# Optimization experiments

Measured on AMD Instinct MI355X. Metric: run time of the kernel, lower is better.

The kernel has to match this reference:

```python
import jax, jax.numpy as jnp
import numpy as np

B, S, D = 2, 2048, 2048
H, G = 32, 8            # n_heads, n_kv_groups
HD = D // H             # head_dim = 64
GS = H // G             # group_size = 4


def _rope(t, cos, sin):
    # t: (B, h, S, HD); cos/sin: (S, HD), start_pos = 0
    half = t.shape[-1] // 2
    rot = jnp.concatenate([-t[..., half:], t[..., :half]], axis=-1)
    return t * cos[None, None] + rot * sin[None, None]


def setup_inputs() -> dict:
    key = jax.random.key(0)
    ks = jax.random.split(key, 7)
    x = jax.random.normal(ks[0], (B, S, D), jnp.float32)
    cos = jax.random.normal(ks[1], (S, HD), jnp.float32)
    sin = jax.random.normal(ks[2], (S, HD), jnp.float32)
    mask = jnp.zeros((S, S), jnp.bool_)
    Wq = jax.random.normal(ks[3], (D, D), jnp.float32) * 0.02
    Wk = jax.random.normal(ks[4], (G * HD, D), jnp.float32) * 0.02
    Wv = jax.random.normal(ks[5], (G * HD, D), jnp.float32) * 0.02
    Wo = jax.random.normal(ks[6], (D, D), jnp.float32) * 0.02
    return {"x": x, "cos": cos, "sin": sin, "mask": mask,
            "Wq": Wq, "Wk": Wk, "Wv": Wv, "Wo": Wo}


def reference(x, cos, sin, mask, Wq, Wk, Wv, Wo):
    b, s, d = x.shape
    # projections (nn.Linear: y = x @ W.T)
    q = (x @ Wq.T).reshape(b, s, H, HD).transpose(0, 2, 1, 3)   # (b,H,s,HD)
    k = (x @ Wk.T).reshape(b, s, G, HD).transpose(0, 2, 1, 3)   # (b,G,s,HD)
    v = (x @ Wv.T).reshape(b, s, G, HD).transpose(0, 2, 1, 3)   # (b,G,s,HD)
    q = _rope(q, cos, sin)
    k = _rope(k, cos, sin)
    # GQA: heads grouped contiguously per kv group (equivalent to repeat_interleave on kv)
    qg = q.reshape(b, G, GS, s, HD)
    scores = jnp.einsum('bgmsd,bgtd->bgmst', qg, k) / jnp.sqrt(jnp.float32(HD))
    # NOTE: original calls non-inplace masked_fill and DISCARDS the result,
    # so the mask has no effect on the output; reproduced faithfully.
    attn = jax.nn.softmax(scores, axis=-1)
    y = jnp.einsum('bgmst,bgtd->bgmsd', attn, v)
    y = y.reshape(b, H, s, HD).transpose(0, 2, 1, 3).reshape(b, s, d)
    return y @ Wo.T
```

## Files before the change

### kernel.cpp

```cpp
#include <hip/hip_runtime.h>
#include <hip/hip_bf16.h>
#include <stdint.h>

#define B_ 2
#define S_ 2048
#define D_ 2048
#define H_ 32
#define G_ 8
#define HD_ 64
#define KVD (G_*HD_)

typedef unsigned short u16;
typedef unsigned int u32;
typedef __attribute__((ext_vector_type(8))) short s8v;
typedef __attribute__((ext_vector_type(4))) float f4v;
typedef __attribute__((ext_vector_type(4))) unsigned int u4v;

static __device__ __forceinline__ float bf2f(u16 u){ return __uint_as_float(((u32)u)<<16); }
static __device__ __forceinline__ u16 f2bf(float f){
  u32 b = __float_as_uint(f);
  return (u16)((b + 0x7FFFu + ((b>>16)&1u)) >> 16);
}
static __device__ __forceinline__ u32 pk2bf(float a, float b){
  float2 f2 = make_float2(a, b);
  __hip_bfloat162 h = __float22bfloat162_rn(f2);
  return *(u32*)&h;
}

struct CvtArgs {
  const float *x, *wq, *wk, *wv, *wo;
  u16 *xb, *wqkvb, *wob;
};
__global__ void k_cvt5(CvtArgs a){
  const int E0 = 2097152;
  const int E1 = E0 + 1048576;
  const int E2 = E1 + 262144;
  const int E3 = E2 + 262144;
  const int E4 = E3 + 1048576;
  int u = blockIdx.x*blockDim.x + threadIdx.x;
  int stride = gridDim.x*blockDim.x;
  for (; u < E4; u += stride){
    const float* s; u16* d; int off;
    if      (u < E0){ s = a.x;  d = a.xb;               off = u; }
    else if (u < E1){ s = a.wq; d = a.wqkvb;            off = u - E0; }
    else if (u < E2){ s = a.wk; d = a.wqkvb + 4194304;  off = u - E1; }
    else if (u < E3){ s = a.wv; d = a.wqkvb + 5242880;  off = u - E2; }
    else            { s = a.wo; d = a.wob;              off = u - E3; }
    float4 f = *(const float4*)(s + (long)off*4);
    uint2 o;
    o.x = (u32)f2bf(f.x) | ((u32)f2bf(f.y)<<16);
    o.y = (u32)f2bf(f.z) | ((u32)f2bf(f.w)<<16);
    *(uint2*)(d + (long)off*4) = o;
  }
}

template<int MODE>
__global__ __launch_bounds__(256) void k_gemm(const u16* __restrict__ A,
    const u16* __restrict__ Bw,
    void* __restrict__ C, void* __restrict__ C2, void* __restrict__ C3,
    const float* __restrict__ cs, const float* __restrict__ sn,
    int N_unused, int K){
  __shared__ u16 As[128*32];
  __shared__ u16 Bs[128*32];
  const int tid = threadIdx.x;
  const int lane = tid & 63, wid = tid >> 6;
  const int l15 = lane & 15, l4 = lane >> 4;
  const int wr = wid >> 1, wc = wid & 1;
  const long Arow0 = (long)blockIdx.x * 128;
  const long Brow0 = (long)blockIdx.y * 128;
  f4v acc[4][4] = {};
  for (int k0 = 0; k0 < K; k0 += 32){
    if (k0) __syncthreads();
    #pragma unroll
    for (int is = 0; is < 2; ++is){
      int c = (is*4 + wid)*64 + lane;
      int row = c >> 2, slot = c & 3;
      int ko = slot ^ (row & 3);
      const u16* srcA = A + (Arow0 + row)*K + k0 + ko*8;
      const u16* srcB = Bw + (Brow0 + row)*K + k0 + ko*8;
      __builtin_amdgcn_global_load_lds((__attribute__((address_space(1))) void*)(void*)srcA,
          (__attribute__((address_space(3))) void*)(As + (is*4 + wid)*512), 16, 0, 0);
      __builtin_amdgcn_global_load_lds((__attribute__((address_space(1))) void*)(void*)srcB,
          (__attribute__((address_space(3))) void*)(Bs + (is*4 + wid)*512), 16, 0, 0);
    }
    __syncthreads();
    s8v af[4], bf[4];
    #pragma unroll
    for (int m = 0; m < 4; ++m){
      int row = wr*64 + m*16 + l15;
      af[m] = *(const s8v*)((const char*)As + row*64 + ((l4 ^ (row & 3))<<4));
    }
    #pragma unroll
    for (int n = 0; n < 4; ++n){
      int col = wc*64 + n*16 + l15;
      bf[n] = *(const s8v*)((const char*)Bs + col*64 + ((l4 ^ (col & 3))<<4));
    }
    #pragma unroll
    for (int m = 0; m < 4; ++m)
      #pragma unroll
      for (int n = 0; n < 4; ++n)
        acc[m][n] = __builtin_amdgcn_mfma_f32_16x16x32_bf16(af[m], bf[n], acc[m][n], 0, 0, 0);
  }

  if (MODE == 0){
    #pragma unroll
    for (int m = 0; m < 4; ++m)
      #pragma unroll
      for (int n = 0; n < 4; ++n)
        #pragma unroll
        for (int i = 0; i < 4; ++i){
          long r = Arow0 + wr*64 + m*16 + l4*4 + i;
          long c = Brow0 + wc*64 + n*16 + l15;
          ((float*)C)[r*2048 + c] = acc[m][n][i];
        }
  } else {
    const long col0 = Brow0 + wc*64;
    if (col0 < 2560){
      u16* out; long cbase; int stride; float qs;
      if (col0 < 2048){ out = (u16*)C;  cbase = col0;        stride = 2048; qs = 0.125f*1.44269504f; }
      else            { out = (u16*)C2; cbase = col0 - 2048; stride = 512;  qs = 1.0f; }
      #pragma unroll
      for (int m = 0; m < 4; ++m){
        long r0 = Arow0 + wr*64 + m*16 + l4*4;
        #pragma unroll
        for (int i = 0; i < 4; ++i){
          int s = (int)((r0 + i) & (S_-1));
          const float* cb = cs + s*64 + l15;
          const float* sb = sn + s*64 + l15;
          #pragma unroll
          for (int n = 0; n < 2; ++n){
            float c0 = cb[n*16],      s0v = sb[n*16];
            float c1 = cb[n*16 + 32], s1v = sb[n*16 + 32];
            float t0 = acc[m][n][i], t1 = acc[m][n+2][i];
            long cA = cbase + n*16 + l15;
            out[(r0+i)*stride + cA]      = f2bf((t0*c0 - t1*s0v)*qs);
            out[(r0+i)*stride + cA + 32] = f2bf((t1*c1 + t0*s1v)*qs);
          }
        }
      }
    } else {
      u16* vt = (u16*)C3;
      int g = (int)((col0 - 2560) >> 6);
      #pragma unroll
      for (int m = 0; m < 4; ++m){
        long r0 = Arow0 + wr*64 + m*16 + l4*4;
        int b = (int)(r0 >> 11), s0 = (int)(r0 & (S_-1));
        #pragma unroll
        for (int n = 0; n < 4; ++n){
          int d = n*16 + l15;
          uint2 w;
          w.x = (u32)f2bf(acc[m][n][0]) | ((u32)f2bf(acc[m][n][1])<<16);
          w.y = (u32)f2bf(acc[m][n][2]) | ((u32)f2bf(acc[m][n][3])<<16);
          *(uint2*)(vt + ((long)(b*G_ + g)*64 + d)*S_ + s0) = w;
        }
      }
    }
  }
}

__global__ __launch_bounds__(512) void k_fattn(const u16* __restrict__ q,
    const u16* __restrict__ k, const u16* __restrict__ vt, u16* __restrict__ o){
  __shared__ u16 Ks[2][64*64];
  __shared__ u16 VTs[2][64*64];
  __shared__ u16 Ps[8][32*64];
  const int tid = threadIdx.x, lane = tid & 63, wid = tid >> 6;
  const int l15 = lane & 15, l4 = lane >> 4;
  const int qt = blockIdx.x, h = blockIdx.y, b = blockIdx.z;
  const int g = h >> 2;
  const long qrow0 = (long)b*S_ + qt*256 + wid*32;

  s8v aq[2][2];
  #pragma unroll
  for (int mf = 0; mf < 2; ++mf)
    #pragma unroll
    for (int kf = 0; kf < 2; ++kf)
      aq[mf][kf] = *(const s8v*)(q + (qrow0 + mf*16 + l15)*D_ + h*64 + kf*32 + l4*8);

  u4v ov; ov.x = ov.y = ov.z = ov.w = 0x3F803F80u;
  const s8v ones = *(s8v*)&ov;

  const int c = wid*64 + lane;
  const int srow = c >> 3, ko = (c & 7) ^ (srow & 7);
  const u16* ksrc0 = k  + ((long)b*S_ + srow)*KVD + g*64 + ko*8;
  const u16* vsrc0 = vt + ((long)(b*G_ + g)*64 + srow)*S_ + ko*8;

  auto stage = [&](int kt){
    int bsel = kt & 1;
    __builtin_amdgcn_global_load_lds(
        (__attribute__((address_space(1))) void*)(void*)(ksrc0 + (long)kt*64*KVD),
        (__attribute__((address_space(3))) void*)(&Ks[bsel][wid*512]), 16, 0, 0);
    __builtin_amdgcn_global_load_lds(
        (__attribute__((address_space(1))) void*)(void*)(vsrc0 + kt*64),
        (__attribute__((address_space(3))) void*)(&VTs[bsel][wid*512]), 16, 0, 0);
  };

  f4v oacc[2][4] = {};
  f4v lsacc[2] = {};

  stage(0);
  for (int kt = 0; kt < S_/64; ++kt){
    __syncthreads();
    if (kt + 1 < S_/64) stage(kt + 1);
    const u16* KsB = Ks[kt & 1];
    const u16* VsB = VTs[kt & 1];

    s8v bk[4][2];
    #pragma unroll
    for (int nf = 0; nf < 4; ++nf){
      int key = nf*16 + l15;
      #pragma unroll
      for (int kf = 0; kf < 2; ++kf)
        bk[nf][kf] = *(const s8v*)((const char*)KsB + key*128 + (((kf*4 + l4) ^ (key & 7))<<4));
    }
    f4v sacc[2][4] = {};
    __builtin_amdgcn_s_setprio(1);
    #pragma unroll
    for (int mf = 0; mf < 2; ++mf)
      #pragma unroll
      for (int nf = 0; nf < 4; ++nf)
        #pragma unroll
        for (int kf = 0; kf < 2; ++kf)
          sacc[mf][nf] = __builtin_amdgcn_mfma_f32_16x16x32_bf16(bk[nf][kf], aq[mf][kf], sacc[mf][nf], 0, 0, 0);
    __builtin_amdgcn_s_setprio(0);

    #pragma unroll
    for (int mf = 0; mf < 2; ++mf){
      int r = mf*16 + l15;
      char* pbase = (char*)Ps[wid] + r*128 + (l4 & 1)*8;
      #pragma unroll
      for (int nf = 0; nf < 4; ++nf){
        float p0 = __builtin_amdgcn_exp2f(sacc[mf][nf][0]);
        float p1 = __builtin_amdgcn_exp2f(sacc[mf][nf][1]);
        float p2 = __builtin_amdgcn_exp2f(sacc[mf][nf][2]);
        float p3 = __builtin_amdgcn_exp2f(sacc[mf][nf][3]);
        uint2 w; w.x = pk2bf(p0, p1); w.y = pk2bf(p2, p3);
        int slot = nf*2 + (l4 >> 1);
        *(uint2*)(pbase + ((slot ^ (r & 7))<<4)) = w;
      }
    }

    s8v ap[2][2];
    #pragma unroll
    for (int mf = 0; mf < 2; ++mf){
      int r = mf*16 + l15;
      #pragma unroll
      for (int kf = 0; kf < 2; ++kf)
        ap[mf][kf] = *(const s8v*)((const char*)Ps[wid] + r*128 + (((kf*4 + l4) ^ (r & 7))<<4));
    }
    __builtin_amdgcn_s_setprio(1);
    #pragma unroll
    for (int mf = 0; mf < 2; ++mf)
      #pragma unroll
      for (int kf = 0; kf < 2; ++kf)
        lsacc[mf] = __builtin_amdgcn_mfma_f32_16x16x32_bf16(ap[mf][kf], ones, lsacc[mf], 0, 0, 0);
    #pragma unroll
    for (int nd = 0; nd < 4; ++nd){
      int d = nd*16 + l15;
      #pragma unroll
      for (int kf = 0; kf < 2; ++kf){
        s8v bv = *(const s8v*)((const char*)VsB + d*128 + (((kf*4 + l4) ^ (d & 7))<<4));
        #pragma unroll
        for (int mf = 0; mf < 2; ++mf)
          oacc[mf][nd] = __builtin_amdgcn_mfma_f32_16x16x32_bf16(ap[mf][kf], bv, oacc[mf][nd], 0, 0, 0);
      }
    }
    __builtin_amdgcn_s_setprio(0);
  }

  #pragma unroll
  for (int mf = 0; mf < 2; ++mf){
    f4v li;
    #pragma unroll
    for (int i = 0; i < 4; ++i) li[i] = 1.f / lsacc[mf][i];
    #pragma unroll
    for (int nd = 0; nd < 4; ++nd){
      long r = qrow0 + mf*16 + l4*4;
      int cc = h*64 + nd*16 + l15;
      o[(r+0)*D_ + cc] = f2bf(oacc[mf][nd][0]*li[0]);
      o[(r+1)*D_ + cc] = f2bf(oacc[mf][nd][1]*li[1]);
      o[(r+2)*D_ + cc] = f2bf(oacc[mf][nd][2]*li[2]);
      o[(r+3)*D_ + cc] = f2bf(oacc[mf][nd][3]*li[3]);
    }
  }
}

extern "C" void kernel_launch(void* const* d_in, const int* in_sizes, int n_in,
                              void* d_out, int out_size, void* d_ws, size_t ws_size,
                              hipStream_t stream){
  const float* x    = (const float*)d_in[0];
  const float* cosp = (const float*)d_in[1];
  const float* sinp = (const float*)d_in[2];
  const float* Wq = (const float*)d_in[4];
  const float* Wk = (const float*)d_in[5];
  const float* Wv = (const float*)d_in[6];
  const float* Wo = (const float*)d_in[7];

  char* ws = (char*)d_ws;
  size_t off = 0;
  auto alloc = [&](size_t bytes)->char*{
    char* p = ws + off; off += (bytes + 255) & ~(size_t)255; return p;
  };
  u16* xb    = (u16*)alloc((size_t)8388608*2);
  u16* wqkvb = (u16*)alloc((size_t)6291456*2);
  u16* wob   = (u16*)alloc((size_t)4194304*2);
  u16* qb    = (u16*)alloc((size_t)8388608*2);
  u16* kb    = (u16*)alloc((size_t)2097152*2);
  u16* vtb   = (u16*)alloc((size_t)2097152*2);
  u16* ab    = (u16*)alloc((size_t)8388608*2);
  if (ws_size < off) return;

  CvtArgs ca{ x, Wq, Wk, Wv, Wo, xb, wqkvb, wob };
  k_cvt5<<<2048,256,0,stream>>>(ca);

  k_gemm<3><<<dim3(32,24,1),256,0,stream>>>(xb, wqkvb, qb, kb, vtb, cosp, sinp, 3072, 2048);

  k_fattn<<<dim3(8,32,2),512,0,stream>>>(qb, kb, vtb, ab);

  k_gemm<0><<<dim3(32,16,1),256,0,stream>>>(ab, wob, d_out, nullptr, nullptr, nullptr, nullptr, 2048, 2048);
}
```

Before: 230.7 us.

## Double-buffer LDS tiles in GEMM and prefetch next K-stage during MFMA

```diff
diff --git a/kernel.cpp b/kernel.cpp
--- a/kernel.cpp
+++ b/kernel.cpp
@@ -60,46 +60,63 @@
     void* __restrict__ C, void* __restrict__ C2, void* __restrict__ C3,
     const float* __restrict__ cs, const float* __restrict__ sn,
     int N_unused, int K){
-  __shared__ u16 As[128*32];
-  __shared__ u16 Bs[128*32];
+  __shared__ u16 As[2][128*32];
+  __shared__ u16 Bs[2][128*32];
   const int tid = threadIdx.x;
   const int lane = tid & 63, wid = tid >> 6;
   const int l15 = lane & 15, l4 = lane >> 4;
   const int wr = wid >> 1, wc = wid & 1;
   const long Arow0 = (long)blockIdx.x * 128;
   const long Brow0 = (long)blockIdx.y * 128;
+  const int NKS = K >> 5;
+
+  const u16* srcA0[2]; const u16* srcB0[2];
+  #pragma unroll
+  for (int is = 0; is < 2; ++is){
+    int c = (is*4 + wid)*64 + lane;
+    int row = c >> 2, slot = c & 3;
+    int ko = slot ^ (row & 3);
+    srcA0[is] = A  + (Arow0 + row)*K + ko*8;
+    srcB0[is] = Bw + (Brow0 + row)*K + ko*8;
+  }
+  auto stage = [&](int ks){
+    int bsel = ks & 1, k0 = ks << 5;
+    #pragma unroll
+    for (int is = 0; is < 2; ++is){
+      __builtin_amdgcn_global_load_lds(
+          (__attribute__((address_space(1))) void*)(void*)(srcA0[is] + k0),
+          (__attribute__((address_space(3))) void*)(&As[bsel][(is*4 + wid)*512]), 16, 0, 0);
+      __builtin_amdgcn_global_load_lds(
+          (__attribute__((address_space(1))) void*)(void*)(srcB0[is] + k0),
+          (__attribute__((address_space(3))) void*)(&Bs[bsel][(is*4 + wid)*512]), 16, 0, 0);
+    }
+  };
+
   f4v acc[4][4] = {};
-  for (int k0 = 0; k0 < K; k0 += 32){
-    if (k0) __syncthreads();
-    #pragma unroll
-    for (int is = 0; is < 2; ++is){
-      int c = (is*4 + wid)*64 + lane;
-      int row = c >> 2, slot = c & 3;
-      int ko = slot ^ (row & 3);
-      const u16* srcA = A + (Arow0 + row)*K + k0 + ko*8;
-      const u16* srcB = Bw + (Brow0 + row)*K + k0 + ko*8;
-      __builtin_amdgcn_global_load_lds((__attribute__((address_space(1))) void*)(void*)srcA,
-          (__attribute__((address_space(3))) void*)(As + (is*4 + wid)*512), 16, 0, 0);
-      __builtin_amdgcn_global_load_lds((__attribute__((address_space(1))) void*)(void*)srcB,
-          (__attribute__((address_space(3))) void*)(Bs + (is*4 + wid)*512), 16, 0, 0);
-    }
+  stage(0);
+  for (int ks = 0; ks < NKS; ++ks){
     __syncthreads();
+    if (ks + 1 < NKS) stage(ks + 1);
+    const u16* AsB = As[ks & 1];
+    const u16* BsB = Bs[ks & 1];
     s8v af[4], bf[4];
     #pragma unroll
     for (int m = 0; m < 4; ++m){
       int row = wr*64 + m*16 + l15;
-      af[m] = *(const s8v*)((const char*)As + row*64 + ((l4 ^ (row & 3))<<4));
+      af[m] = *(const s8v*)((const char*)AsB + row*64 + ((l4 ^ (row & 3))<<4));
     }
     #pragma unroll
     for (int n = 0; n < 4; ++n){
       int col = wc*64 + n*16 + l15;
-      bf[n] = *(const s8v*)((const char*)Bs + col*64 + ((l4 ^ (col & 3))<<4));
-    }
+      bf[n] = *(const s8v*)((const char*)BsB + col*64 + ((l4 ^ (col & 3))<<4));
+    }
+    __builtin_amdgcn_s_setprio(1);
     #pragma unroll
     for (int m = 0; m < 4; ++m)
       #pragma unroll
       for (int n = 0; n < 4; ++n)
         acc[m][n] = __builtin_amdgcn_mfma_f32_16x16x32_bf16(af[m], bf[n], acc[m][n], 0, 0, 0);
+    __builtin_amdgcn_s_setprio(0);
   }
 
   if (MODE == 0){
```

Result: no change. 231.6 us (+0.4%).
